# Performance work log

Measured on AMD Instinct MI355X. Metric: run time of the kernel, lower is better.

## Reference

```python
import jax, jax.numpy as jnp
import numpy as np

KH, KW = 3, 3
STRIDE = (1, 1)
PAD = (1, 1)
DIL = (1, 1)

def _unfold(x, kh, kw, stride, padding, dilation):
    # Faithful torch.nn.functional.unfold: output (B, C*kh*kw, L) with
    # feature ordering channel-slowest, then kh, then kw.
    B, C, H, W = x.shape
    h_out = (H + 2 * padding[0] - dilation[0] * (kh - 1) - 1) // stride[0] + 1
    w_out = (W + 2 * padding[1] - dilation[1] * (kw - 1) - 1) // stride[1] + 1
    xp = jnp.pad(x, ((0, 0), (0, 0), (padding[0], padding[0]), (padding[1], padding[1])))
    rows = []
    for i in range(kh):  # small fixed kernel loop (9 slices), not a data-dim loop
        for j in range(kw):
            r0 = i * dilation[0]
            c0 = j * dilation[1]
            patch = xp[:, :, r0:r0 + h_out * stride[0]:stride[0],
                             c0:c0 + w_out * stride[1]:stride[1]]  # (B,C,h_out,w_out)
            rows.append(patch)
    # stack -> (B, C, kh*kw, h_out, w_out); reorder so feature dim = C*kh*kw
    p = jnp.stack(rows, axis=2)
    p = p.reshape(B, C * kh * kw, h_out * w_out)
    return p, h_out, w_out

def transform_transposed_unfolded_input(inp_unf):
    # Default hook: identity (as in the base class).
    return inp_unf

def reference(x, weight, bias):
    B = x.shape[0]
    O = weight.shape[0]
    inp_unf, h_out, w_out = _unfold(x, KH, KW, STRIDE, PAD, DIL)   # (B, C*k*k, L)
    inp_t = jnp.swapaxes(inp_unf, 1, 2)                            # (B, L, C*k*k)
    inp_t = transform_transposed_unfolded_input(inp_t)
    w2d = weight.reshape(O, -1)                                    # (O, C*k*k)
    out_unf = jnp.einsum('blk,ok->bol', inp_t, w2d)                # (B, O, L)
    out = out_unf.reshape(B, O, h_out, w_out)
    out = out + bias.reshape(1, O, 1, 1)
    return out

def setup_inputs() -> dict:
    key = jax.random.key(0)
    k1, k2, k3 = jax.random.split(key, 3)
    x = jax.random.normal(k1, (32, 128, 56, 56), dtype=jnp.float32)
    fan_in = 128 * KH * KW
    weight = jax.random.normal(k2, (256, 128, KH, KW), dtype=jnp.float32) / np.sqrt(fan_in)
    bias = jax.random.normal(k3, (256,), dtype=jnp.float32) * 0.01
    return {"x": x, "weight": weight, "bias": bias}
```

## Files before the change

kernel.cpp:

```cpp
#include <hip/hip_runtime.h>
#include <hip/hip_bf16.h>
#include <cstdint>

typedef float f32x4 __attribute__((ext_vector_type(4)));
typedef short bf16x8 __attribute__((ext_vector_type(8)));
typedef short short8 __attribute__((ext_vector_type(8)));

#define CIN   128
#define WIMG  56
#define HWSZ  3136
#define OCH   256
#define HP    58
#define WP    58

__global__ void small_prep(const float* __restrict__ wsrc,
                           __hip_bfloat16* __restrict__ wb,
                           __hip_bfloat16* __restrict__ xb) {
    int bidx = blockIdx.x;
    if (bidx < 456) {
        int idx = bidx * 256 + threadIdx.x;
        int c8  = idx & 15;
        int t   = idx >> 4;
        int b   = t / 228;
        int pos = t - b * 228;
        int h, w;
        if (pos < 58)       { h = 0;             w = pos; }
        else if (pos < 116) { h = 57;            w = pos - 58; }
        else if (pos < 172) { h = pos - 116 + 1; w = 0; }
        else                { h = pos - 172 + 1; w = 57; }
        uint4 z = {0, 0, 0, 0};
        *(uint4*)((char*)xb + (((size_t)(b * HP + h) * WP + w) * CIN + c8 * 8) * 2) = z;
    } else {
        int idx = (bidx - 456) * 256 + threadIdx.x;
        int c    = idx & 127;
        int rest = idx >> 7;
        int o    = rest & 255;
        int ij   = rest >> 8;
        wb[idx] = __float2bfloat16(wsrc[((size_t)o * CIN + c) * 9 + ij]);
    }
}

__global__ __launch_bounds__(256)
void cast_transpose_x(const float* __restrict__ x,
                      __hip_bfloat16* __restrict__ xb) {
    __shared__ float tile[64][33];
    const int hw0 = blockIdx.x * 32;
    const int c0  = blockIdx.y * 64;
    const int b   = blockIdx.z;

    const int lx = threadIdx.x & 31;
    const int lc = threadIdx.x >> 5;
    const float* src = x + ((size_t)(b * CIN + c0 + lc) * HWSZ) + hw0 + lx;
#pragma unroll
    for (int k = 0; k < 8; ++k)
        tile[lc + k * 8][lx] = src[(size_t)(k * 8) * HWSZ];
    __syncthreads();

    const int slot = threadIdx.x & 7;
    const int hwl  = threadIdx.x >> 3;
    int hw = hw0 + hwl;
    int h = hw / WIMG;
    int w = hw - h * WIMG;
    short8 v;
#pragma unroll
    for (int j = 0; j < 8; ++j) {
        __hip_bfloat16 hb = __float2bfloat16(tile[slot * 8 + j][hwl]);
        v[j] = *reinterpret_cast<short*>(&hb);
    }
    *(short8*)(xb + (((size_t)b * HP + (h + 1)) * WP + (w + 1)) * CIN + c0 + slot * 8) = v;
}

__device__ __forceinline__ void gload16(const void* g, void* l) {
    __builtin_amdgcn_global_load_lds(
        (const __attribute__((address_space(1))) unsigned*)g,
        (__attribute__((address_space(3))) unsigned*)l,
        16, 0, 0);
}

__global__ __launch_bounds__(512, 2)
void conv_gemm(const __hip_bfloat16* __restrict__ xb,
               const __hip_bfloat16* __restrict__ wb,
               const float* __restrict__ bias,
               float* __restrict__ out) {
    extern __shared__ __attribute__((aligned(16))) char smem[];

    const int tid = threadIdx.x;
    const int wv  = tid >> 6;
    const int ln  = tid & 63;

    int bid = blockIdx.x;
    bid = (bid & 7) * 56 + (bid >> 3);
    const int b   = bid / 14;
    const int rg  = bid - b * 14;
    const int m0  = b * HWSZ + rg * 224;
    const int h0  = rg * 4;

#pragma unroll
    for (int r = 0; r < 11; ++r) {
        int li = r * 512 + tid;
        if (li < 5568) {
            int pix  = li >> 4;
            int slot = li & 15;
            int lr = pix / 58;
            int lc2 = pix - lr * 58;
            const char* src = (const char*)xb +
                ((((size_t)(b * HP + h0 + lr)) * WP + lc2) << 8) +
                ((slot ^ (pix & 7)) << 4);
            gload16(src, smem + (li << 4));
        }
    }

    const int wm  = wv >> 2;
    const int wn  = wv & 3;
    const int fr  = ln & 15;
    const int kby = (ln >> 4) * 16;

    int lpixI[7];
#pragma unroll
    for (int mi = 0; mi < 7; ++mi) {
        int lp = wm * 112 + mi * 16 + fr;
        int lh = lp / 56;
        int lw = lp - lh * 56;
        lpixI[mi] = lh * 58 + lw;
    }

    const __hip_bfloat16* bbase = wb + (wn * 64 + fr) * CIN + ((ln >> 4) << 3);

    f32x4 acc[7][4] = {};
    bf16x8 bqA[4][2], bqB[4][2];

#define LOADB(dst, toff) do {                                                 \
    _Pragma("unroll") for (int ni = 0; ni < 4; ++ni)                          \
    _Pragma("unroll") for (int kk = 0; kk < 2; ++kk)                          \
        dst[ni][kk] = *(const bf16x8*)(bbase + (toff) + ni*(16*CIN) + kk*32); \
} while (0)

#define TAP(tapoff, ckb, bq) do {                                             \
    _Pragma("unroll") for (int kk = 0; kk < 2; ++kk)                          \
    _Pragma("unroll") for (int mi = 0; mi < 7; ++mi) {                        \
        int px = lpixI[mi] + (tapoff);                                        \
        bf16x8 afr = *(const bf16x8*)(smem + (px << 8) +                      \
                     (((ckb) + kk*64 + kby) ^ ((px & 7) << 4)));              \
        _Pragma("unroll") for (int ni = 0; ni < 4; ++ni)                      \
            acc[mi][ni] = __builtin_amdgcn_mfma_f32_16x16x32_bf16(            \
                afr, bq[ni][kk], acc[mi][ni], 0, 0, 0);                       \
    }                                                                         \
} while (0)

    __syncthreads();

    LOADB(bqA, 0);
#pragma unroll 1
    for (int i = 0; i < 9; ++i) {
        const int ii = i / 3, jj = i - 3 * ii;
        const int tapoff = ii * 58 + jj;
        const int offB   = i * (OCH * CIN);

        LOADB(bqB, offB + 64);
        TAP(tapoff, 0, bqA);
        if (i < 8) LOADB(bqA, offB + OCH * CIN);
        TAP(tapoff, 128, bqB);
    }
#undef LOADB
#undef TAP

    const int laneR4 = (ln >> 4) * 4;
    float bn[4];
#pragma unroll
    for (int ni = 0; ni < 4; ++ni)
        bn[ni] = bias[wn * 64 + ni * 16 + fr];

#pragma unroll
    for (int mi = 0; mi < 7; ++mi) {
        int p0 = m0 + wm * 112 + mi * 16 + laneR4;
        int hw = p0 - b * HWSZ;
#pragma unroll
        for (int ni = 0; ni < 4; ++ni) {
            int n = wn * 64 + ni * 16 + fr;
            float4 v;
            v.x = acc[mi][ni][0] + bn[ni];
            v.y = acc[mi][ni][1] + bn[ni];
            v.z = acc[mi][ni][2] + bn[ni];
            v.w = acc[mi][ni][3] + bn[ni];
            *(float4*)(out + ((size_t)(b * OCH + n) * HWSZ + hw)) = v;
        }
    }
}

extern "C" void kernel_launch(void* const* d_in, const int* in_sizes, int n_in,
                              void* d_out, int out_size, void* d_ws, size_t ws_size,
                              hipStream_t stream) {
    const float* x    = (const float*)d_in[0];
    const float* w    = (const float*)d_in[1];
    const float* bias = (const float*)d_in[2];
    float* out = (float*)d_out;

    char* ws = (char*)d_ws;
    __hip_bfloat16* xbuf = (__hip_bfloat16*)ws;
    __hip_bfloat16* wbuf = (__hip_bfloat16*)(ws + 27557888);

    hipFuncSetAttribute(reinterpret_cast<const void*>(conv_gemm),
                        hipFuncAttributeMaxDynamicSharedMemorySize, 89088);

    small_prep<<<1608, 256, 0, stream>>>(w, wbuf, xbuf);
    cast_transpose_x<<<dim3(98, 2, 32), dim3(256), 0, stream>>>(x, xbuf);
    conv_gemm<<<448, 512, 89088, stream>>>(xbuf, wbuf, bias, out);
}
```

Measured before the change: 108.7 us.

## Software-pipeline LDS A-fragment loads with MFMA across K sub-chunks and taps

Splits each tap's 128-channel K into four 32-wide chunks and double-buffers both the A fragments read from LDS and the B fragments read from global memory. The next chunk's reads are issued before the current chunk's MFMAs, including prefetching the next tap's first chunk. The LDS swizzle key changes from pixel index to image column, so keys can be computed from lw+jj without a per-read multiply. The aim is to hide LDS and global load latency behind matrix math, at the cost of more registers for buffered A fragments, which could reduce occupancy at 2 blocks per SM or cause spills.

New measurement: 110.1 us. No clear change (+1.4%).

```diff
diff --git a/kernel.cpp b/kernel.cpp
--- a/kernel.cpp
+++ b/kernel.cpp
@@ -105,7 +105,7 @@
             int lc2 = pix - lr * 58;
             const char* src = (const char*)xb +
                 ((((size_t)(b * HP + h0 + lr)) * WP + lc2) << 8) +
-                ((slot ^ (pix & 7)) << 4);
+                ((slot ^ (lc2 & 7)) << 4);
             gload16(src, smem + (li << 4));
         }
     }
@@ -115,54 +115,86 @@
     const int fr  = ln & 15;
     const int kby = (ln >> 4) * 16;
 
-    int lpixI[7];
+    int lpixI[7], lwv[7];
 #pragma unroll
     for (int mi = 0; mi < 7; ++mi) {
         int lp = wm * 112 + mi * 16 + fr;
         int lh = lp / 56;
         int lw = lp - lh * 56;
         lpixI[mi] = lh * 58 + lw;
+        lwv[mi]   = lw;
     }
 
     const __hip_bfloat16* bbase = wb + (wn * 64 + fr) * CIN + ((ln >> 4) << 3);
 
     f32x4 acc[7][4] = {};
-    bf16x8 bqA[4][2], bqB[4][2];
-
-#define LOADB(dst, toff) do {                                                 \
+    bf16x8 afA[7], afB[7], bqA[4], bqB[4];
+
+#define LOADB4(dst, toff) do {                                                \
     _Pragma("unroll") for (int ni = 0; ni < 4; ++ni)                          \
-    _Pragma("unroll") for (int kk = 0; kk < 2; ++kk)                          \
-        dst[ni][kk] = *(const bf16x8*)(bbase + (toff) + ni*(16*CIN) + kk*32); \
+        dst[ni] = *(const bf16x8*)(bbase + (toff) + ni * (16 * CIN));         \
 } while (0)
 
-#define TAP(tapoff, ckb, bq) do {                                             \
-    _Pragma("unroll") for (int kk = 0; kk < 2; ++kk)                          \
+#define DS7(dst, tapoff, colb, keyarr) do {                                   \
     _Pragma("unroll") for (int mi = 0; mi < 7; ++mi) {                        \
         int px = lpixI[mi] + (tapoff);                                        \
-        bf16x8 afr = *(const bf16x8*)(smem + (px << 8) +                      \
-                     (((ckb) + kk*64 + kby) ^ ((px & 7) << 4)));              \
-        _Pragma("unroll") for (int ni = 0; ni < 4; ++ni)                      \
-            acc[mi][ni] = __builtin_amdgcn_mfma_f32_16x16x32_bf16(            \
-                afr, bq[ni][kk], acc[mi][ni], 0, 0, 0);                       \
+        dst[mi] = *(const bf16x8*)(smem + (px << 8) +                         \
+                                   (((colb) + kby) ^ keyarr[mi]));            \
     }                                                                         \
 } while (0)
 
+#define MM28(af, bq) do {                                                     \
+    _Pragma("unroll") for (int mi = 0; mi < 7; ++mi)                          \
+    _Pragma("unroll") for (int ni = 0; ni < 4; ++ni)                          \
+        acc[mi][ni] = __builtin_amdgcn_mfma_f32_16x16x32_bf16(                \
+            af[mi], bq[ni], acc[mi][ni], 0, 0, 0);                            \
+} while (0)
+
     __syncthreads();
 
-    LOADB(bqA, 0);
+    int key7[7];
+#pragma unroll
+    for (int mi = 0; mi < 7; ++mi) key7[mi] = (lwv[mi] & 7) << 4;
+    DS7(afA, 0, 0, key7);
+    LOADB4(bqA, 0);
+
 #pragma unroll 1
     for (int i = 0; i < 9; ++i) {
         const int ii = i / 3, jj = i - 3 * ii;
         const int tapoff = ii * 58 + jj;
         const int offB   = i * (OCH * CIN);
-
-        LOADB(bqB, offB + 64);
-        TAP(tapoff, 0, bqA);
-        if (i < 8) LOADB(bqA, offB + OCH * CIN);
-        TAP(tapoff, 128, bqB);
-    }
-#undef LOADB
-#undef TAP
+        const bool pf = (i < 8);
+
+#pragma unroll
+        for (int mi = 0; mi < 7; ++mi) key7[mi] = ((lwv[mi] + jj) & 7) << 4;
+
+        DS7(afB, tapoff, 64, key7);
+        LOADB4(bqB, offB + 32);
+        MM28(afA, bqA);
+
+        DS7(afA, tapoff, 128, key7);
+        LOADB4(bqA, offB + 64);
+        MM28(afB, bqB);
+
+        DS7(afB, tapoff, 192, key7);
+        LOADB4(bqB, offB + 96);
+        MM28(afA, bqA);
+
+        if (pf) {
+            const int i2  = i + 1;
+            const int ii2 = i2 / 3, jj2 = i2 - 3 * ii2;
+            const int tapoffN = ii2 * 58 + jj2;
+            int keyN[7];
+#pragma unroll
+            for (int mi = 0; mi < 7; ++mi) keyN[mi] = ((lwv[mi] + jj2) & 7) << 4;
+            DS7(afA, tapoffN, 0, keyN);
+            LOADB4(bqA, offB + OCH * CIN);
+        }
+        MM28(afB, bqB);
+    }
+#undef LOADB4
+#undef DS7
+#undef MM28
 
     const int laneR4 = (ln >> 4) * 4;
     float bn[4];
```
